# Kernel optimization log

Hardware: AMD Instinct MI355X
Metric: run time of the kernel (lower is better)

Reference implementation:

```python
import jax, jax.numpy as jnp
import numpy as np

SFREQ = 100

def _std1(x, axis):
    # torch.std default: unbiased (ddof=1)
    return jnp.std(x, axis=axis, ddof=1)

def setup_inputs() -> dict:
    key = jax.random.key(0)
    eeg_data = jax.random.normal(key, (2048, 128, 500), dtype=jnp.float32)
    return {"eeg_data": eeg_data}

def reference(eeg_data):
    B, C, T = eeg_data.shape
    # --- P300 window: [T//3, 2T//3) ---
    p0, p1 = T // 3, 2 * T // 3
    p300 = eeg_data[:, :, p0:p1]                      # (B,C,Wp)
    peak_idx = jnp.argmax(p300, axis=-1)              # (B,C)
    lat = (p0 + peak_idx).astype(eeg_data.dtype) / SFREQ  # (B,C)
    amp = jnp.max(p300, axis=-1)                      # (B,C)
    p300_feats = jnp.stack([
        lat.mean(axis=1), _std1(lat, 1),
        amp.mean(axis=1), amp.max(axis=1),
        (amp * lat).mean(axis=1),
    ], axis=1)                                        # (B,5)
    # --- N200 window: [0.2T, 0.35T) ---
    n0, n1 = int(0.2 * T), int(0.35 * T)
    n2_amp = jnp.min(eeg_data[:, :, n0:n1], axis=-1)  # (B,C)
    n2_feats = jnp.stack([
        n2_amp.mean(axis=1), _std1(n2_amp, 1), n2_amp.min(axis=1),
    ], axis=1)                                        # (B,3)
    # --- alpha (prestim) power: [0, T//3) ---
    alpha_p = jnp.mean(eeg_data[:, :, :p0] ** 2, axis=-1)  # (B,C)
    alpha_feats = jnp.stack([
        alpha_p.mean(axis=1), _std1(alpha_p, 1), alpha_p.max(axis=1),
    ], axis=1)                                        # (B,3)
    # --- beta (motor) power: [T//3, 2T//3) ---
    beta_p = jnp.mean(p300 ** 2, axis=-1)             # (B,C)
    beta_feats = jnp.stack([
        beta_p.mean(axis=1), _std1(beta_p, 1),
    ], axis=1)                                        # (B,2)
    return jnp.concatenate([p300_feats, n2_feats, alpha_feats, beta_feats], axis=1)  # (B,13)
```

## Files before the change

kernel.cpp:

```cpp
#include <hip/hip_runtime.h>
#include <float.h>

#define NCH  128
#define TLEN 500
#define P0 166
#define P1 333
#define N0 100
#define N1 175

template<int CTRL>
__device__ __forceinline__ float dpp_rorf(float v) {
    const int s = __float_as_int(v);
    const int d = __builtin_amdgcn_update_dpp(s, s, CTRL, 0xF, 0xF, false);
    return __int_as_float(d);
}
template<int CTRL>
__device__ __forceinline__ int dpp_rori(int v) {
    return __builtin_amdgcn_update_dpp(v, v, CTRL, 0xF, 0xF, false);
}

__device__ __forceinline__ float wave_sum(float v) {
#pragma unroll
    for (int m = 32; m; m >>= 1) v += __shfl_xor(v, m, 64);
    return v;
}
__device__ __forceinline__ float wave_min(float v) {
#pragma unroll
    for (int m = 32; m; m >>= 1) v = fminf(v, __shfl_xor(v, m, 64));
    return v;
}
__device__ __forceinline__ float wave_max(float v) {
#pragma unroll
    for (int m = 32; m; m >>= 1) v = fmaxf(v, __shfl_xor(v, m, 64));
    return v;
}

__global__ __launch_bounds__(256) void erp_feats_kernel(
    const float* __restrict__ eeg, float* __restrict__ out) {
    const int b    = blockIdx.x;
    const int tid  = threadIdx.x;
    const int wid  = tid >> 6;
    const int lane = tid & 63;
    const int g    = lane >> 4;
    const int l    = lane & 15;

    __shared__ float s_lat[NCH], s_amp[NCH], s_n2[NCH], s_alpha[NCH], s_beta[NCH];

    const float* __restrict__ base = eeg + (size_t)b * NCH * TLEN;

#pragma unroll 1
    for (int p = 0; p < 8; ++p) {
        const int c = p * 16 + wid * 4 + g;
        const float* __restrict__ ch = base + (size_t)c * TLEN;

        float asum  = 0.0f;
        float bsum  = 0.0f;
        float n2min = FLT_MAX;
        float pmax  = -FLT_MAX;
        int   pidx  = P0;

#pragma unroll
        for (int k = 0; k < 5; ++k) {
            const int i = k * 16 + l;
            const float4 v = *reinterpret_cast<const float4*>(ch + 4 * i);
            const float e[4] = {v.x, v.y, v.z, v.w};
            const int t0 = 4 * i;
#pragma unroll
            for (int j = 0; j < 4; ++j) {
                const int t = t0 + j;
                const float x  = e[j];
                const float xx = x * x;
                if (t < P0) {
                    asum += xx;
                } else {
                    bsum += xx;
                    if (x > pmax) { pmax = x; pidx = t; }
                }
                if (t >= N0 && t < N1) n2min = fminf(n2min, x);
            }
        }
        if (l < 4) {
            const int i = 80 + l;
            const float4 v = *reinterpret_cast<const float4*>(ch + 4 * i);
            const float e[4] = {v.x, v.y, v.z, v.w};
            const int t0 = 4 * i;
#pragma unroll
            for (int j = 0; j < 4; ++j) {
                const int t = t0 + j;
                if (t < P1) {
                    const float x = e[j];
                    bsum += x * x;
                    if (x > pmax) { pmax = x; pidx = t; }
                }
            }
        }

#define RED_STEP(CTRL)                                                       \
        {                                                                    \
            asum  += dpp_rorf<CTRL>(asum);                                   \
            bsum  += dpp_rorf<CTRL>(bsum);                                   \
            n2min  = fminf(n2min, dpp_rorf<CTRL>(n2min));                    \
            const float om = dpp_rorf<CTRL>(pmax);                           \
            const int   oi = dpp_rori<CTRL>(pidx);                           \
            if (om > pmax || (om == pmax && oi < pidx)) { pmax = om; pidx = oi; } \
        }
        RED_STEP(0x128)
        RED_STEP(0x124)
        RED_STEP(0x122)
        RED_STEP(0x121)
#undef RED_STEP

        if (l == 0) {
            s_lat[c]   = (float)pidx / 100.0f;
            s_amp[c]   = pmax;
            s_n2[c]    = n2min;
            s_alpha[c] = asum / 166.0f;
            s_beta[c]  = bsum / 167.0f;
        }
    }

    __syncthreads();

    if (wid == 0) {
        const float lat0 = s_lat[lane],   lat1 = s_lat[lane + 64];
        const float amp0 = s_amp[lane],   amp1 = s_amp[lane + 64];
        const float n20  = s_n2[lane],    n21  = s_n2[lane + 64];
        const float al0  = s_alpha[lane], al1  = s_alpha[lane + 64];
        const float be0  = s_beta[lane],  be1  = s_beta[lane + 64];

        const float inv_n = 1.0f / 128.0f;
        const float inv_m = 1.0f / 127.0f;

        const float lat_mean = wave_sum(lat0 + lat1) * inv_n;
        const float amp_mean = wave_sum(amp0 + amp1) * inv_n;
        const float n2_mean  = wave_sum(n20 + n21)   * inv_n;
        const float al_mean  = wave_sum(al0 + al1)   * inv_n;
        const float be_mean  = wave_sum(be0 + be1)   * inv_n;
        const float axl_mean = wave_sum(amp0 * lat0 + amp1 * lat1) * inv_n;

        const float dl0 = lat0 - lat_mean, dl1 = lat1 - lat_mean;
        const float lat_std = sqrtf(wave_sum(dl0 * dl0 + dl1 * dl1) * inv_m);
        const float dn0 = n20 - n2_mean, dn1 = n21 - n2_mean;
        const float n2_std = sqrtf(wave_sum(dn0 * dn0 + dn1 * dn1) * inv_m);
        const float da0 = al0 - al_mean, da1 = al1 - al_mean;
        const float al_std = sqrtf(wave_sum(da0 * da0 + da1 * da1) * inv_m);
        const float db0 = be0 - be_mean, db1 = be1 - be_mean;
        const float be_std = sqrtf(wave_sum(db0 * db0 + db1 * db1) * inv_m);

        const float amp_max = wave_max(fmaxf(amp0, amp1));
        const float n2_min  = wave_min(fminf(n20, n21));
        const float al_max  = wave_max(fmaxf(al0, al1));

        if (lane == 0) {
            float* o = out + (size_t)b * 13;
            o[0]  = lat_mean;
            o[1]  = lat_std;
            o[2]  = amp_mean;
            o[3]  = amp_max;
            o[4]  = axl_mean;
            o[5]  = n2_mean;
            o[6]  = n2_std;
            o[7]  = n2_min;
            o[8]  = al_mean;
            o[9]  = al_std;
            o[10] = al_max;
            o[11] = be_mean;
            o[12] = be_std;
        }
    }
}

extern "C" void kernel_launch(void* const* d_in, const int* in_sizes, int n_in,
                              void* d_out, int out_size, void* d_ws, size_t ws_size,
                              hipStream_t stream) {
    const float* eeg = (const float*)d_in[0];
    float* out = (float*)d_out;
    const int B = in_sizes[0] / (NCH * TLEN);
    erp_feats_kernel<<<dim3(B), dim3(256), 0, stream>>>(eeg, out);
}
```

Before: 72.39 us.

## Double-buffer channel loads across passes and specialize per-segment window logic

Replaces the rolled 8-pass channel loop with a manually unrolled software pipeline that issues the next pass's float4 loads into a second register set while the current pass is being reduced. The per-element window tests are also specialized per float4 segment, so most segments no longer carry time-index comparisons, and the accumulations use fma. The intent is to keep more memory requests in flight per wave and hide global load latency in this bandwidth-bound kernel. It costs roughly twice the register footprint for staged loads, which could lower occupancy.

Result: no change. 72.20 us (-0.3%).

```diff
diff --git a/kernel.cpp b/kernel.cpp
--- a/kernel.cpp
+++ b/kernel.cpp
@@ -4,9 +4,6 @@
 #define NCH  128
 #define TLEN 500
 #define P0 166
-#define P1 333
-#define N0 100
-#define N1 175
 
 template<int CTRL>
 __device__ __forceinline__ float dpp_rorf(float v) {
@@ -33,6 +30,104 @@
 #pragma unroll
     for (int m = 32; m; m >>= 1) v = fmaxf(v, __shfl_xor(v, m, 64));
     return v;
+}
+
+__device__ __forceinline__ void compute_pass(
+    float4 s0, float4 s1, float4 s2, float4 s3, float4 s4, float4 s5,
+    int c, int l, int l4, bool lt4,
+    float* __restrict__ s_lat, float* __restrict__ s_amp, float* __restrict__ s_n2,
+    float* __restrict__ s_alpha, float* __restrict__ s_beta) {
+
+    float asum  = 0.0f;
+    float bsum  = 0.0f;
+    float n2min = FLT_MAX;
+    float pmax  = -FLT_MAX;
+    int   pidx  = 0x7fffffff;
+
+#define PMAXU(x, t) { if ((x) > pmax) { pmax = (x); pidx = (t); } }
+
+    {
+        const float e[4] = {s0.x, s0.y, s0.z, s0.w};
+#pragma unroll
+        for (int j = 0; j < 4; ++j) asum = fmaf(e[j], e[j], asum);
+    }
+    {
+        const float e[4] = {s1.x, s1.y, s1.z, s1.w};
+#pragma unroll
+        for (int j = 0; j < 4; ++j) asum = fmaf(e[j], e[j], asum);
+        if (l >= 9) {
+            n2min = fminf(n2min, fminf(fminf(e[0], e[1]), fminf(e[2], e[3])));
+        }
+    }
+    {
+        const float e[4] = {s2.x, s2.y, s2.z, s2.w};
+#pragma unroll
+        for (int j = 0; j < 4; ++j) {
+            const int u = l4 + j;
+            const float x = e[j];
+            if (u < 38) {
+                asum = fmaf(x, x, asum);
+            } else {
+                bsum = fmaf(x, x, bsum);
+                PMAXU(x, 128 + u);
+            }
+            if (u < 47) n2min = fminf(n2min, x);
+        }
+    }
+    {
+        const float e[4] = {s3.x, s3.y, s3.z, s3.w};
+#pragma unroll
+        for (int j = 0; j < 4; ++j) {
+            const float x = e[j];
+            bsum = fmaf(x, x, bsum);
+            PMAXU(x, 192 + l4 + j);
+        }
+    }
+    {
+        const float e[4] = {s4.x, s4.y, s4.z, s4.w};
+#pragma unroll
+        for (int j = 0; j < 4; ++j) {
+            const float x = e[j];
+            bsum = fmaf(x, x, bsum);
+            PMAXU(x, 256 + l4 + j);
+        }
+    }
+    if (lt4) {
+        const float e[4] = {s5.x, s5.y, s5.z, s5.w};
+#pragma unroll
+        for (int j = 0; j < 4; ++j) {
+            const int u = l4 + j;
+            if (u < 13) {
+                const float x = e[j];
+                bsum = fmaf(x, x, bsum);
+                PMAXU(x, 320 + u);
+            }
+        }
+    }
+#undef PMAXU
+
+#define RED_STEP(CTRL)                                                        \
+    {                                                                         \
+        asum  += dpp_rorf<CTRL>(asum);                                        \
+        bsum  += dpp_rorf<CTRL>(bsum);                                        \
+        n2min  = fminf(n2min, dpp_rorf<CTRL>(n2min));                         \
+        const float om = dpp_rorf<CTRL>(pmax);                                \
+        const int   oi = dpp_rori<CTRL>(pidx);                                \
+        if (om > pmax || (om == pmax && oi < pidx)) { pmax = om; pidx = oi; } \
+    }
+    RED_STEP(0x128)
+    RED_STEP(0x124)
+    RED_STEP(0x122)
+    RED_STEP(0x121)
+#undef RED_STEP
+
+    if (l == 0) {
+        s_lat[c]   = (float)pidx / 100.0f;
+        s_amp[c]   = pmax;
+        s_n2[c]    = n2min;
+        s_alpha[c] = asum / 166.0f;
+        s_beta[c]  = bsum / 167.0f;
+    }
 }
 
 __global__ __launch_bounds__(256) void erp_feats_kernel(
@@ -43,81 +138,43 @@
     const int lane = tid & 63;
     const int g    = lane >> 4;
     const int l    = lane & 15;
+    const int l4   = l << 2;
+    const bool lt4 = (l < 4);
+    const int cbase = (wid << 2) + g;
 
     __shared__ float s_lat[NCH], s_amp[NCH], s_n2[NCH], s_alpha[NCH], s_beta[NCH];
 
     const float* __restrict__ base = eeg + (size_t)b * NCH * TLEN;
 
-#pragma unroll 1
-    for (int p = 0; p < 8; ++p) {
-        const int c = p * 16 + wid * 4 + g;
-        const float* __restrict__ ch = base + (size_t)c * TLEN;
-
-        float asum  = 0.0f;
-        float bsum  = 0.0f;
-        float n2min = FLT_MAX;
-        float pmax  = -FLT_MAX;
-        int   pidx  = P0;
-
-#pragma unroll
-        for (int k = 0; k < 5; ++k) {
-            const int i = k * 16 + l;
-            const float4 v = *reinterpret_cast<const float4*>(ch + 4 * i);
-            const float e[4] = {v.x, v.y, v.z, v.w};
-            const int t0 = 4 * i;
-#pragma unroll
-            for (int j = 0; j < 4; ++j) {
-                const int t = t0 + j;
-                const float x  = e[j];
-                const float xx = x * x;
-                if (t < P0) {
-                    asum += xx;
-                } else {
-                    bsum += xx;
-                    if (x > pmax) { pmax = x; pidx = t; }
-                }
-                if (t >= N0 && t < N1) n2min = fminf(n2min, x);
-            }
-        }
-        if (l < 4) {
-            const int i = 80 + l;
-            const float4 v = *reinterpret_cast<const float4*>(ch + 4 * i);
-            const float e[4] = {v.x, v.y, v.z, v.w};
-            const int t0 = 4 * i;
-#pragma unroll
-            for (int j = 0; j < 4; ++j) {
-                const int t = t0 + j;
-                if (t < P1) {
-                    const float x = e[j];
-                    bsum += x * x;
-                    if (x > pmax) { pmax = x; pidx = t; }
-                }
-            }
-        }
-
-#define RED_STEP(CTRL)                                                       \
-        {                                                                    \
-            asum  += dpp_rorf<CTRL>(asum);                                   \
-            bsum  += dpp_rorf<CTRL>(bsum);                                   \
-            n2min  = fminf(n2min, dpp_rorf<CTRL>(n2min));                    \
-            const float om = dpp_rorf<CTRL>(pmax);                           \
-            const int   oi = dpp_rori<CTRL>(pidx);                           \
-            if (om > pmax || (om == pmax && oi < pidx)) { pmax = om; pidx = oi; } \
-        }
-        RED_STEP(0x128)
-        RED_STEP(0x124)
-        RED_STEP(0x122)
-        RED_STEP(0x121)
-#undef RED_STEP
-
-        if (l == 0) {
-            s_lat[c]   = (float)pidx / 100.0f;
-            s_amp[c]   = pmax;
-            s_n2[c]    = n2min;
-            s_alpha[c] = asum / 166.0f;
-            s_beta[c]  = bsum / 167.0f;
-        }
-    }
+#define ISSUE(d, P)                                                           \
+    {                                                                         \
+        const float* __restrict__ _ch = base + (size_t)((P) * 16 + cbase) * TLEN; \
+        d##0 = *reinterpret_cast<const float4*>(_ch + l4);                    \
+        d##1 = *reinterpret_cast<const float4*>(_ch +  64 + l4);              \
+        d##2 = *reinterpret_cast<const float4*>(_ch + 128 + l4);              \
+        d##3 = *reinterpret_cast<const float4*>(_ch + 192 + l4);              \
+        d##4 = *reinterpret_cast<const float4*>(_ch + 256 + l4);              \
+        if (lt4) d##5 = *reinterpret_cast<const float4*>(_ch + 320 + l4);     \
+    }
+#define DO_COMPUTE(d, P)                                                      \
+    compute_pass(d##0, d##1, d##2, d##3, d##4, d##5, (P) * 16 + cbase,        \
+                 l, l4, lt4, s_lat, s_amp, s_n2, s_alpha, s_beta);
+
+    float4 a0, a1, a2, a3, a4, a5{};
+    float4 b0, b1, b2, b3, b4, b5{};
+
+    ISSUE(a, 0)
+    ISSUE(b, 1) DO_COMPUTE(a, 0)
+    ISSUE(a, 2) DO_COMPUTE(b, 1)
+    ISSUE(b, 3) DO_COMPUTE(a, 2)
+    ISSUE(a, 4) DO_COMPUTE(b, 3)
+    ISSUE(b, 5) DO_COMPUTE(a, 4)
+    ISSUE(a, 6) DO_COMPUTE(b, 5)
+    ISSUE(b, 7) DO_COMPUTE(a, 6)
+    DO_COMPUTE(b, 7)
+
+#undef ISSUE
+#undef DO_COMPUTE
 
     __syncthreads();
 
```
